# Kernel optimization log

Hardware: AMD Instinct MI355X
Metric: run time of the kernel (lower is better)

## Reference

```python
import jax, jax.numpy as jnp
import numpy as np

B, S, E, H = 4, 2048, 2048, 16
D = E // H  # head_dim = 128
ROPE_BASE = 10000.0


def rope(x, base=ROPE_BASE, offset=0):
    # x: (..., seq, d) with interleaved even/odd rotation
    d = x.shape[-1]
    s = x.shape[-2]
    inv_freq = base ** (-jnp.arange(0, d, 2, dtype=jnp.float32) / d)  # (d/2,)
    pos = jnp.arange(offset, s + offset, dtype=jnp.float32)  # (s,)
    ang = pos[:, None] * inv_freq  # (s, d/2)
    sin, cos = jnp.sin(ang), jnp.cos(ang)
    xe, xo = x[..., 0::2], x[..., 1::2]
    re = xe * cos - xo * sin
    ro = xe * sin + xo * cos
    return jnp.stack([re, ro], axis=-1).reshape(x.shape)


def setup_inputs() -> dict:
    key = jax.random.key(0)
    ks = jax.random.split(key, 9)
    w = lambda k, shp: jax.random.normal(k, shp, dtype=jnp.float32) * 0.02
    return {
        "x": jax.random.normal(ks[0], (B, S, E), dtype=jnp.float32),
        "Wq": w(ks[1], (E, E)), "bq": w(ks[2], (E,)),
        "Wk": w(ks[3], (E, E)), "bk": w(ks[4], (E,)),
        "Wv": w(ks[5], (E, E)), "bv": w(ks[6], (E,)),
        "Wo": w(ks[7], (E, E)), "bo": w(ks[8], (E,)),
    }


def reference(x, Wq, bq, Wk, bk, Wv, bv, Wo, bo):
    b, s, _ = x.shape
    scale = D ** -0.5
    # torch Linear: y = x @ W.T + b
    def proj(W, bias):
        y = jnp.einsum('bse,fe->bsf', x, W) + bias
        return y.reshape(b, s, H, D).transpose(0, 2, 1, 3)  # (b, h, s, d)
    q = rope(proj(Wq, bq))
    k = rope(proj(Wk, bk))
    v = proj(Wv, bv)
    attn = jnp.einsum('bhqd,bhkd->bhqk', q, k) * scale  # (b, h, s, s)
    causal = jnp.triu(jnp.ones((s, s), dtype=bool), k=1)
    attn = jnp.where(causal, -jnp.inf, attn)
    attn_weights = jax.nn.softmax(attn, axis=-1)
    out = jnp.einsum('bhqk,bhkd->bhqd', attn_weights, v)
    out = out.transpose(0, 2, 1, 3).reshape(b, s, E)
    return jnp.einsum('bse,fe->bsf', out, Wo) + bo
```

## Files before the change

kernel.cpp:

```cpp
#include <hip/hip_runtime.h>
#include <hip/hip_bf16.h>
#include <stdint.h>

#define B_ 4
#define S_ 2048
#define E_ 2048
#define H_ 16
#define D_ 128
#define M_ (B_ * S_)

typedef unsigned short ushort_t;
typedef unsigned int uint_t;
typedef __attribute__((ext_vector_type(4))) float f32x4;
typedef __attribute__((ext_vector_type(2))) uint_t u32x2;
typedef __attribute__((ext_vector_type(8))) short bf16x8;

__device__ __forceinline__ ushort_t f2bf(float f) {
  uint_t u = __float_as_uint(f);
  u += 0x7FFFu + ((u >> 16) & 1u);
  return (ushort_t)(u >> 16);
}
__device__ __forceinline__ float bf2f(ushort_t h) {
  return __uint_as_float(((uint_t)h) << 16);
}
__device__ __forceinline__ uint_t cvt_pk_bf16(float lo, float hi) {
  uint_t r;
  asm("v_cvt_pk_bf16_f32 %0, %1, %2" : "=v"(r) : "v"(lo), "v"(hi));
  return r;
}

#define GLOAD_LDS16(gp, lp)                                   \
  __builtin_amdgcn_global_load_lds(                           \
      (__attribute__((address_space(1))) void*)(gp),          \
      (__attribute__((address_space(3))) void*)(lp), 16, 0, 0)

__global__ void f32_to_bf16(const float* __restrict__ in, ushort_t* __restrict__ out,
                            size_t n4) {
  const size_t stride = (size_t)gridDim.x * blockDim.x;
  for (size_t i = (size_t)blockIdx.x * blockDim.x + threadIdx.x; i < n4; i += stride) {
    const f32x4 f = __builtin_nontemporal_load((const f32x4*)in + i);
    u32x2 o;
    o[0] = (uint_t)f2bf(f[0]) | ((uint_t)f2bf(f[1]) << 16);
    o[1] = (uint_t)f2bf(f[2]) | ((uint_t)f2bf(f[3]) << 16);
    __builtin_nontemporal_store(o, (u32x2*)out + i);
  }
}

__global__ void rope_table(float2* __restrict__ tab) {
  const int i = blockIdx.x * 256 + threadIdx.x;
  const int s = i >> 6, p = i & 63;
  const float inv = exp2f(-0.20762050593046f * (float)p);
  float sn, cs;
  sincosf((float)s * inv, &sn, &cs);
  tab[i] = make_float2(cs, sn);
}

__global__ __launch_bounds__(256) void transpose_v(const ushort_t* __restrict__ Vp,
                                                   ushort_t* __restrict__ Vt) {
  const int b = blockIdx.z, h = blockIdx.y;
  const int s0 = blockIdx.x * 64;
  const int tid = threadIdx.x;
  __shared__ ushort_t T[64][136];
#pragma unroll
  for (int i = 0; i < 4; i++) {
    const int c = i * 256 + tid;
    const int s = c >> 4, d8 = c & 15;
    *(bf16x8*)(&T[s][d8 * 8]) =
        *(const bf16x8*)(Vp + (size_t)(b * S_ + s0 + s) * E_ + h * D_ + d8 * 8);
  }
  __syncthreads();
#pragma unroll
  for (int i = 0; i < 4; i++) {
    const int c = i * 256 + tid;
    const int d = c >> 3, s8 = c & 7;
    bf16x8 v;
#pragma unroll
    for (int j = 0; j < 8; j++) v[j] = (short)T[s8 * 8 + j][d];
    *(bf16x8*)(Vt + ((size_t)(b * H_ + h) * D_ + d) * S_ + s0 + s8 * 8) = v;
  }
}

template <int MODE>
__global__ __launch_bounds__(512, 2) void gemm8p(const ushort_t* __restrict__ A,
                                                 const ushort_t* __restrict__ Bw,
                                                 const float* __restrict__ bias,
                                                 const float2* __restrict__ tab,
                                                 void* __restrict__ Cv) {
  __shared__ __align__(16) char lds[131072];
  const int tid = threadIdx.x;
  const int w = tid >> 6, l = tid & 63, g = l >> 4, ln = l & 15;
  const int wm = w >> 2, wn = w & 3;

  const int flat = blockIdx.x;
  const int swz = (flat & 7) * 32 + (flat >> 3);
  const int m0 = (swz >> 3) * 256, n0 = (swz & 7) * 256;

  const ushort_t* Ab = A + (size_t)m0 * E_;
  const ushort_t* Bb = Bw + (size_t)n0 * E_;

  int srcRow[2], srcCc[2];
#pragma unroll
  for (int i = 0; i < 2; i++) {
    const int c = i * 512 + tid;
    const int r2 = c >> 3;
    const int j = (c & 7) ^ (r2 & 7);
    srcRow[i] = 2 * r2 + (j >> 2);
    srcCc[i] = (j & 3) * 8;
  }

  auto STAGE = [&](int t_, int mat, int kk) {
    char* dst = lds + (t_ & 1) * 65536 + mat * 32768 + kk * 16384;
    const ushort_t* src = mat ? Bb : Ab;
#pragma unroll
    for (int i = 0; i < 2; i++)
      GLOAD_LDS16(src + (size_t)srcRow[i] * E_ + t_ * 64 + kk * 32 + srcCc[i],
                  dst + (i * 512 + w * 64) * 16);
  };

  const int rp = ln >> 1;
  const int chunkl = ((((ln & 1) << 2) | g) ^ rp);
  const int aBase = wm * 8192 + rp * 128 + chunkl * 16;
  const int bBase = 32768 + wn * 4096 + rp * 128 + chunkl * 16;

  f32x4 acc[8][4];
#pragma unroll
  for (int mi = 0; mi < 8; mi++)
#pragma unroll
    for (int ni = 0; ni < 4; ni++)
#pragma unroll
      for (int r = 0; r < 4; r++) acc[mi][ni][r] = 0.f;

#define BARR asm volatile("s_barrier" ::: "memory")
#define VM6 asm volatile("s_waitcnt vmcnt(6)" ::: "memory")
#define VM0 asm volatile("s_waitcnt vmcnt(0)" ::: "memory")
#define LGKM0                                            \
  do {                                                   \
    asm volatile("s_waitcnt lgkmcnt(0)" ::: "memory");   \
    __builtin_amdgcn_sched_barrier(0);                   \
  } while (0)
#define PH_RDB(bp, kk)                                                         \
  _Pragma("unroll") for (int ni = 0; ni < 4; ni++) bfr[ni] =                   \
      *(const bf16x8*)((bp) + bBase + (kk)*16384 + ni * 1024);
#define PH_RDA(bp, kk, mh)                                                     \
  _Pragma("unroll") for (int ai = 0; ai < 4; ai++) af[ai] =                    \
      *(const bf16x8*)((bp) + aBase + (kk)*16384 + (mh)*4096 + ai * 1024);
#define PH_MM(mh)                                                              \
  __builtin_amdgcn_s_setprio(1);                                               \
  _Pragma("unroll") for (int ai = 0; ai < 4; ai++)                             \
      _Pragma("unroll") for (int ni = 0; ni < 4; ni++) acc[(mh)*4 + ai][ni] =  \
          __builtin_amdgcn_mfma_f32_16x16x32_bf16(af[ai], bfr[ni],             \
                                                  acc[(mh)*4 + ai][ni], 0, 0, 0); \
  __builtin_amdgcn_s_setprio(0);

  STAGE(0, 1, 0); STAGE(0, 0, 0); STAGE(0, 1, 1); STAGE(0, 0, 1);
  STAGE(1, 1, 0); STAGE(1, 0, 0); STAGE(1, 1, 1);
  VM6;
  BARR;

  const char* b0 = lds;
  const char* b1 = lds + 65536;
  bf16x8 af[4], bfr[4];

  for (int it = 0; it < 15; ++it) {
    const int t2 = 2 * it;
    PH_RDB(b0, 0); PH_RDA(b0, 0, 0); STAGE(t2 + 1, 0, 1); BARR; LGKM0; PH_MM(0); BARR;
    PH_RDA(b0, 0, 1);                STAGE(t2 + 2, 1, 0); BARR; LGKM0; PH_MM(1); BARR;
    PH_RDB(b0, 1); PH_RDA(b0, 1, 0); STAGE(t2 + 2, 0, 0); BARR; LGKM0; PH_MM(0); BARR;
    PH_RDA(b0, 1, 1);                STAGE(t2 + 2, 1, 1); BARR; LGKM0; PH_MM(1); VM6; BARR;
    PH_RDB(b1, 0); PH_RDA(b1, 0, 0); STAGE(t2 + 2, 0, 1); BARR; LGKM0; PH_MM(0); BARR;
    PH_RDA(b1, 0, 1);                STAGE(t2 + 3, 1, 0); BARR; LGKM0; PH_MM(1); BARR;
    PH_RDB(b1, 1); PH_RDA(b1, 1, 0); STAGE(t2 + 3, 0, 0); BARR; LGKM0; PH_MM(0); BARR;
    PH_RDA(b1, 1, 1);                STAGE(t2 + 3, 1, 1); BARR; LGKM0; PH_MM(1); VM6; BARR;
  }
  PH_RDB(b0, 0); PH_RDA(b0, 0, 0); STAGE(31, 0, 1); BARR; LGKM0; PH_MM(0); BARR;
  PH_RDA(b0, 0, 1);                                 BARR; LGKM0; PH_MM(1); BARR;
  PH_RDB(b0, 1); PH_RDA(b0, 1, 0);                  BARR; LGKM0; PH_MM(0); BARR;
  PH_RDA(b0, 1, 1);                                 BARR; LGKM0; PH_MM(1); VM0; BARR;
  PH_RDB(b1, 0); PH_RDA(b1, 0, 0);                  BARR; LGKM0; PH_MM(0); BARR;
  PH_RDA(b1, 0, 1);                                 BARR; LGKM0; PH_MM(1); BARR;
  PH_RDB(b1, 1); PH_RDA(b1, 1, 0);                  BARR; LGKM0; PH_MM(0); BARR;
  PH_RDA(b1, 1, 1);                                 BARR; LGKM0; PH_MM(1);

#undef PH_MM
#undef PH_RDA
#undef PH_RDB
#undef LGKM0
#undef VM0
#undef VM6
#undef BARR

  float bv[4];
#pragma unroll
  for (int ni = 0; ni < 4; ni++) bv[ni] = bias[n0 + wn * 64 + ni * 16 + ln];
#pragma unroll
  for (int mi = 0; mi < 8; mi++)
#pragma unroll
    for (int ni = 0; ni < 4; ni++) {
      const int col = n0 + wn * 64 + ni * 16 + ln;
      const int p = (col & 127) >> 1;
      const float sgn = (col & 1) ? 1.f : -1.f;
      const int row0 = m0 + wm * 128 + mi * 16 + g * 4;
#pragma unroll
      for (int r = 0; r < 4; r++) {
        const float v = acc[mi][ni][r] + bv[ni];
        if (MODE == 1) {
          ((float*)Cv)[(size_t)(row0 + r) * E_ + col] = v;
        } else if (MODE == 2) {
          const float partner = __shfl_xor(v, 1);
          const float2 t = tab[((row0 + r) & (S_ - 1)) * 64 + p];
          ((ushort_t*)Cv)[(size_t)(row0 + r) * E_ + col] =
              f2bf(v * t.x + sgn * partner * t.y);
        } else {
          ((ushort_t*)Cv)[(size_t)(row0 + r) * E_ + col] = f2bf(v);
        }
      }
    }
}

__global__ __launch_bounds__(256, 2) void attn_fwd(const ushort_t* __restrict__ Q,
                                                   const ushort_t* __restrict__ K,
                                                   const ushort_t* __restrict__ Vt,
                                                   ushort_t* __restrict__ O) {
  const int flat = blockIdx.x;
  const int pair = flat >> 6;
  const int bh = flat & 63;
  const int b = bh >> 4, h = bh & 15;
  const int tid = threadIdx.x;
  const int w = tid >> 6, l = tid & 63, g = l >> 4, ln = l & 15;

  __shared__ ushort_t Ks[2][64 * 128];
  __shared__ ushort_t Vs[2][128 * 64];
  __shared__ ushort_t Ps[4][32 * 64];

  const ushort_t* Kb = K + (size_t)(b * S_) * E_ + h * D_;
  const ushort_t* Vb = Vt + (size_t)(b * H_ + h) * D_ * S_;
  const float scale = 0.08838834764831845f;

#define STAGE_KV(buf, kv0_)                                                      \
  do {                                                                           \
    _Pragma("unroll") for (int i = 0; i < 4; i++) {                              \
      const int c = i * 256 + tid;                                               \
      const int row = c >> 4, sl = c & 15;                                       \
      const int gs = sl ^ (row & 7);                                             \
      GLOAD_LDS16(Kb + (size_t)((kv0_) + row) * E_ + gs * 8,                     \
                  (char*)(&Ks[buf][0]) + (i * 256 + w * 64) * 16);               \
    }                                                                            \
    _Pragma("unroll") for (int i = 0; i < 4; i++) {                              \
      const int c = i * 256 + tid;                                               \
      const int row = c >> 3, sl = c & 7;                                        \
      const int gs = sl ^ (row & 7);                                             \
      GLOAD_LDS16(Vb + (size_t)row * S_ + (kv0_) + gs * 8,                       \
                  (char*)(&Vs[buf][0]) + (i * 256 + w * 64) * 16);               \
    }                                                                            \
  } while (0)

  for (int pass = 0; pass < 2; pass++) {
    const int u = (pass == 0) ? pair : (15 - pair);
    const int q0 = u * 128;
    const int wrow0 = q0 + w * 32;

    bf16x8 qf[2][4];
    {
      const ushort_t* qb = Q + (size_t)(b * S_ + wrow0) * E_ + h * D_;
#pragma unroll
      for (int mi = 0; mi < 2; mi++)
#pragma unroll
        for (int kk = 0; kk < 4; kk++) {
          bf16x8 v = *(const bf16x8*)(qb + (size_t)(mi * 16 + ln) * E_ + kk * 32 + g * 8);
#pragma unroll
          for (int j = 0; j < 8; j++) v[j] = (short)f2bf(bf2f((ushort_t)v[j]) * scale);
          qf[mi][kk] = v;
        }
    }

    f32x4 oacc[2][8];
#pragma unroll
    for (int mi = 0; mi < 2; mi++)
#pragma unroll
      for (int nd = 0; nd < 8; nd++)
#pragma unroll
        for (int r = 0; r < 4; r++) oacc[mi][nd][r] = 0.f;
    float mrun[2], srun[2];
#pragma unroll
    for (int mi = 0; mi < 2; mi++) {
      mrun[mi] = -__builtin_inff();
      srun[mi] = 0.f;
    }

    const int ntu = 2 * u + 2;
    STAGE_KV(0, 0);

    for (int t = 0; t < ntu; t++) {
      const int kv0 = t * 64;
      const int cur = t & 1;
      if (t + 1 < ntu) {
        STAGE_KV(cur ^ 1, kv0 + 64);
        asm volatile("s_waitcnt vmcnt(8)" ::: "memory");
      } else {
        asm volatile("s_waitcnt vmcnt(0)" ::: "memory");
      }
      __builtin_amdgcn_s_barrier();
      __builtin_amdgcn_sched_barrier(0);

      if (kv0 <= wrow0 + 31) {
        const ushort_t* Kst = &Ks[cur][0];
        const ushort_t* Vst = &Vs[cur][0];
        f32x4 sa[2][4];
#pragma unroll
        for (int mi = 0; mi < 2; mi++)
#pragma unroll
          for (int ni = 0; ni < 4; ni++)
#pragma unroll
            for (int r = 0; r < 4; r++) sa[mi][ni][r] = 0.f;
        __builtin_amdgcn_s_setprio(1);
#pragma unroll
        for (int kk = 0; kk < 4; kk++) {
          bf16x8 kf[4];
#pragma unroll
          for (int ni = 0; ni < 4; ni++) {
            const int row = ni * 16 + ln;
            const int sl = (kk * 4 + g) ^ (row & 7);
            kf[ni] = *(const bf16x8*)(Kst + row * 128 + sl * 8);
          }
#pragma unroll
          for (int mi = 0; mi < 2; mi++)
#pragma unroll
            for (int ni = 0; ni < 4; ni++)
              sa[mi][ni] =
                  __builtin_amdgcn_mfma_f32_16x16x32_bf16(kf[ni], qf[mi][kk], sa[mi][ni], 0, 0, 0);
        }
        __builtin_amdgcn_s_setprio(0);
        if (kv0 + 63 > wrow0) {
#pragma unroll
          for (int mi = 0; mi < 2; mi++) {
            const int lim = wrow0 + mi * 16 + ln - kv0;
#pragma unroll
            for (int ni = 0; ni < 4; ni++)
#pragma unroll
              for (int r = 0; r < 4; r++)
                if (ni * 16 + g * 4 + r > lim) sa[mi][ni][r] = -__builtin_inff();
          }
        }
#pragma unroll
        for (int mi = 0; mi < 2; mi++) {
          float vmax = -__builtin_inff();
#pragma unroll
          for (int ni = 0; ni < 4; ni++)
#pragma unroll
            for (int r = 0; r < 4; r++) vmax = fmaxf(vmax, sa[mi][ni][r]);
          vmax = fmaxf(vmax, __shfl_xor(vmax, 16));
          vmax = fmaxf(vmax, __shfl_xor(vmax, 32));
          if (!__all(vmax - mrun[mi] <= 8.0f)) {
            const float mnew = fmaxf(mrun[mi], vmax);
            const float fs = __expf(mrun[mi] - mnew);
            mrun[mi] = mnew;
            srun[mi] *= fs;
#pragma unroll
            for (int nd = 0; nd < 8; nd++)
#pragma unroll
              for (int r = 0; r < 4; r++) oacc[mi][nd][r] *= fs;
          }
          const float m = mrun[mi];
          float psum = 0.f;
#pragma unroll
          for (int ni = 0; ni < 4; ni++) {
            float p0 = __expf(sa[mi][ni][0] - m);
            float p1 = __expf(sa[mi][ni][1] - m);
            float p2 = __expf(sa[mi][ni][2] - m);
            float p3 = __expf(sa[mi][ni][3] - m);
            psum += (p0 + p1) + (p2 + p3);
            const int byteW =
                (((mi * 16 + ln) * 64 + ni * 16 + g * 4) * 2) ^ ((ln & 7) << 4);
            *(uint2*)((char*)(&Ps[w][0]) + byteW) =
                make_uint2(cvt_pk_bf16(p0, p1), cvt_pk_bf16(p2, p3));
          }
          psum += __shfl_xor(psum, 16);
          psum += __shfl_xor(psum, 32);
          srun[mi] += psum;
        }
        asm volatile("s_waitcnt lgkmcnt(0)" ::: "memory");
        __builtin_amdgcn_sched_barrier(0);
        __builtin_amdgcn_s_setprio(1);
#pragma unroll
        for (int ks = 0; ks < 2; ks++) {
          bf16x8 pf[2];
#pragma unroll
          for (int mi = 0; mi < 2; mi++) {
            const int byteR =
                (((mi * 16 + ln) * 64 + ks * 32 + g * 8) * 2) ^ ((ln & 7) << 4);
            pf[mi] = *(const bf16x8*)((const char*)(&Ps[w][0]) + byteR);
          }
#pragma unroll
          for (int nd = 0; nd < 8; nd++) {
            const int row = nd * 16 + ln;
            const int sl = (ks * 4 + g) ^ (row & 7);
            const bf16x8 vf = *(const bf16x8*)(Vst + row * 64 + sl * 8);
#pragma unroll
            for (int mi = 0; mi < 2; mi++)
              oacc[mi][nd] =
                  __builtin_amdgcn_mfma_f32_16x16x32_bf16(vf, pf[mi], oacc[mi][nd], 0, 0, 0);
          }
        }
        __builtin_amdgcn_s_setprio(0);
      }
      __builtin_amdgcn_s_barrier();
    }

    {
      ushort_t* Ob = O + (size_t)(b * S_ + q0 + w * 32) * E_ + h * D_;
#pragma unroll
      for (int mi = 0; mi < 2; mi++) {
        const float inv = 1.0f / srun[mi];
#pragma unroll
        for (int nd = 0; nd < 8; nd++) {
          const uint_t lo = cvt_pk_bf16(oacc[mi][nd][0] * inv, oacc[mi][nd][1] * inv);
          const uint_t hi = cvt_pk_bf16(oacc[mi][nd][2] * inv, oacc[mi][nd][3] * inv);
          *(uint2*)(Ob + (size_t)(mi * 16 + ln) * E_ + nd * 16 + g * 4) = make_uint2(lo, hi);
        }
      }
    }
  }
#undef STAGE_KV
}

extern "C" void kernel_launch(void* const* d_in, const int* in_sizes, int n_in,
                              void* d_out, int out_size, void* d_ws, size_t ws_size,
                              hipStream_t stream) {
  const float* x = (const float*)d_in[0];
  const float* Wq = (const float*)d_in[1];
  const float* bq = (const float*)d_in[2];
  const float* Wk = (const float*)d_in[3];
  const float* bk = (const float*)d_in[4];
  const float* Wv = (const float*)d_in[5];
  const float* bv = (const float*)d_in[6];
  const float* Wo = (const float*)d_in[7];
  const float* bo = (const float*)d_in[8];
  float* out = (float*)d_out;

  ushort_t* ws = (ushort_t*)d_ws;
  const size_t SZ = (size_t)M_ * E_;
  const size_t WSZ = (size_t)E_ * E_;
  ushort_t* xb = ws;
  ushort_t* Qb = ws + SZ;
  ushort_t* Kb = ws + 2 * SZ;
  float2* tbl = (float2*)(ws + 3 * SZ);
  ushort_t* Vb = ws + 3 * SZ;
  ushort_t* Vtb = ws + 4 * SZ;
  ushort_t* Wqb = ws + 5 * SZ;
  ushort_t* Wkb = Wqb + WSZ;
  ushort_t* Wvb = Wkb + WSZ;
  ushort_t* Wob = Wvb + WSZ;
  ushort_t* Ob = xb;

  f32_to_bf16<<<2048, 256, 0, stream>>>(x, xb, SZ / 4);
  f32_to_bf16<<<1024, 256, 0, stream>>>(Wq, Wqb, WSZ / 4);
  f32_to_bf16<<<1024, 256, 0, stream>>>(Wk, Wkb, WSZ / 4);
  f32_to_bf16<<<1024, 256, 0, stream>>>(Wv, Wvb, WSZ / 4);
  f32_to_bf16<<<1024, 256, 0, stream>>>(Wo, Wob, WSZ / 4);
  rope_table<<<512, 256, 0, stream>>>(tbl);

  gemm8p<2><<<256, 512, 0, stream>>>(xb, Wqb, bq, tbl, Qb);
  gemm8p<2><<<256, 512, 0, stream>>>(xb, Wkb, bk, tbl, Kb);
  gemm8p<0><<<256, 512, 0, stream>>>(xb, Wvb, bv, nullptr, Vb);
  transpose_v<<<dim3(32, H_, B_), 256, 0, stream>>>(Vb, Vtb);

  attn_fwd<<<512, 256, 0, stream>>>(Qb, Kb, Vtb, Ob);

  gemm8p<1><<<256, 512, 0, stream>>>(Ob, Wob, bo, nullptr, (void*)out);
}
```

Baseline: 424.2 us.

## Fuse QKV projections into one GEMM launch and use exp2 softmax

Merges the three Q/K/V projection GEMMs into a single 768-block launch that treats the contiguous Wq/Wk/Wv bf16 buffers as one 6144-wide weight matrix, picking bias, output and RoPE handling per column tile. This removes two launch tails and fills the GPU with more concurrent tiles. Separately, attention folds log2(e) into the Q scale and uses the raw v_exp_f32 (exp2) instruction, rescaling the lazy-rescale threshold to match. The rope table moves to a new workspace offset so it no longer aliases the V buffer.

```diff
diff --git a/kernel.cpp b/kernel.cpp
--- a/kernel.cpp
+++ b/kernel.cpp
@@ -26,6 +26,11 @@
 __device__ __forceinline__ uint_t cvt_pk_bf16(float lo, float hi) {
   uint_t r;
   asm("v_cvt_pk_bf16_f32 %0, %1, %2" : "=v"(r) : "v"(lo), "v"(hi));
+  return r;
+}
+__device__ __forceinline__ float fexp2(float x) {
+  float r;
+  asm("v_exp_f32 %0, %1" : "=v"(r) : "v"(x));
   return r;
 }
 
@@ -80,20 +85,77 @@
   }
 }
 
-template <int MODE>
-__global__ __launch_bounds__(512, 2) void gemm8p(const ushort_t* __restrict__ A,
-                                                 const ushort_t* __restrict__ Bw,
-                                                 const float* __restrict__ bias,
-                                                 const float2* __restrict__ tab,
-                                                 void* __restrict__ Cv) {
+#define G8_BARR asm volatile("s_barrier" ::: "memory")
+#define G8_VM6 asm volatile("s_waitcnt vmcnt(6)" ::: "memory")
+#define G8_VM0 asm volatile("s_waitcnt vmcnt(0)" ::: "memory")
+#define G8_LGKM0                                         \
+  do {                                                   \
+    asm volatile("s_waitcnt lgkmcnt(0)" ::: "memory");   \
+    __builtin_amdgcn_sched_barrier(0);                   \
+  } while (0)
+#define G8_RDB(bp, kk)                                                         \
+  _Pragma("unroll") for (int ni = 0; ni < 4; ni++) bfr[ni] =                   \
+      *(const bf16x8*)((bp) + bBase + (kk)*16384 + ni * 1024);
+#define G8_RDA(bp, kk, mh)                                                     \
+  _Pragma("unroll") for (int ai = 0; ai < 4; ai++) af[ai] =                    \
+      *(const bf16x8*)((bp) + aBase + (kk)*16384 + (mh)*4096 + ai * 1024);
+#define G8_MM(mh)                                                              \
+  __builtin_amdgcn_s_setprio(1);                                               \
+  _Pragma("unroll") for (int ai = 0; ai < 4; ai++)                             \
+      _Pragma("unroll") for (int ni = 0; ni < 4; ni++) acc[(mh)*4 + ai][ni] =  \
+          __builtin_amdgcn_mfma_f32_16x16x32_bf16(af[ai], bfr[ni],             \
+                                                  acc[(mh)*4 + ai][ni], 0, 0, 0); \
+  __builtin_amdgcn_s_setprio(0);
+
+#define G8_BODY                                                                              \
+  f32x4 acc[8][4];                                                                           \
+  _Pragma("unroll") for (int mi = 0; mi < 8; mi++)                                           \
+      _Pragma("unroll") for (int ni = 0; ni < 4; ni++)                                       \
+          _Pragma("unroll") for (int r = 0; r < 4; r++) acc[mi][ni][r] = 0.f;                \
+  STAGE(0, 1, 0); STAGE(0, 0, 0); STAGE(0, 1, 1); STAGE(0, 0, 1);                            \
+  STAGE(1, 1, 0); STAGE(1, 0, 0); STAGE(1, 1, 1);                                            \
+  G8_VM6; G8_BARR;                                                                           \
+  const char* b0 = lds;                                                                      \
+  const char* b1 = lds + 65536;                                                              \
+  bf16x8 af[4], bfr[4];                                                                      \
+  for (int it = 0; it < 15; ++it) {                                                          \
+    const int t2 = 2 * it;                                                                   \
+    G8_RDB(b0, 0); G8_RDA(b0, 0, 0); STAGE(t2 + 1, 0, 1); G8_BARR; G8_LGKM0; G8_MM(0); G8_BARR; \
+    G8_RDA(b0, 0, 1);                STAGE(t2 + 2, 1, 0); G8_BARR; G8_LGKM0; G8_MM(1); G8_BARR; \
+    G8_RDB(b0, 1); G8_RDA(b0, 1, 0); STAGE(t2 + 2, 0, 0); G8_BARR; G8_LGKM0; G8_MM(0); G8_BARR; \
+    G8_RDA(b0, 1, 1);                STAGE(t2 + 2, 1, 1); G8_BARR; G8_LGKM0; G8_MM(1); G8_VM6; G8_BARR; \
+    G8_RDB(b1, 0); G8_RDA(b1, 0, 0); STAGE(t2 + 2, 0, 1); G8_BARR; G8_LGKM0; G8_MM(0); G8_BARR; \
+    G8_RDA(b1, 0, 1);                STAGE(t2 + 3, 1, 0); G8_BARR; G8_LGKM0; G8_MM(1); G8_BARR; \
+    G8_RDB(b1, 1); G8_RDA(b1, 1, 0); STAGE(t2 + 3, 0, 0); G8_BARR; G8_LGKM0; G8_MM(0); G8_BARR; \
+    G8_RDA(b1, 1, 1);                STAGE(t2 + 3, 1, 1); G8_BARR; G8_LGKM0; G8_MM(1); G8_VM6; G8_BARR; \
+  }                                                                                          \
+  G8_RDB(b0, 0); G8_RDA(b0, 0, 0); STAGE(31, 0, 1); G8_BARR; G8_LGKM0; G8_MM(0); G8_BARR;    \
+  G8_RDA(b0, 0, 1);                                 G8_BARR; G8_LGKM0; G8_MM(1); G8_BARR;    \
+  G8_RDB(b0, 1); G8_RDA(b0, 1, 0);                  G8_BARR; G8_LGKM0; G8_MM(0); G8_BARR;    \
+  G8_RDA(b0, 1, 1);                                 G8_BARR; G8_LGKM0; G8_MM(1); G8_VM0; G8_BARR; \
+  G8_RDB(b1, 0); G8_RDA(b1, 0, 0);                  G8_BARR; G8_LGKM0; G8_MM(0); G8_BARR;    \
+  G8_RDA(b1, 0, 1);                                 G8_BARR; G8_LGKM0; G8_MM(1); G8_BARR;    \
+  G8_RDB(b1, 1); G8_RDA(b1, 1, 0);                  G8_BARR; G8_LGKM0; G8_MM(0); G8_BARR;    \
+  G8_RDA(b1, 1, 1);                                 G8_BARR; G8_LGKM0; G8_MM(1);
+
+__global__ __launch_bounds__(512, 2) void gemm_qkv(const ushort_t* __restrict__ A,
+                                                   const ushort_t* __restrict__ Bw,
+                                                   const float* __restrict__ bq,
+                                                   const float* __restrict__ bk,
+                                                   const float* __restrict__ bvv,
+                                                   const float2* __restrict__ tab,
+                                                   ushort_t* __restrict__ Qo,
+                                                   ushort_t* __restrict__ Ko,
+                                                   ushort_t* __restrict__ Vo) {
   __shared__ __align__(16) char lds[131072];
   const int tid = threadIdx.x;
   const int w = tid >> 6, l = tid & 63, g = l >> 4, ln = l & 15;
   const int wm = w >> 2, wn = w & 3;
 
   const int flat = blockIdx.x;
-  const int swz = (flat & 7) * 32 + (flat >> 3);
-  const int m0 = (swz >> 3) * 256, n0 = (swz & 7) * 256;
+  const int swz = (flat & 7) * 96 + (flat >> 3);
+  const int mt = swz / 24, nt = swz % 24;
+  const int m0 = mt * 256, n0 = nt * 256;
 
   const ushort_t* Ab = A + (size_t)m0 * E_;
   const ushort_t* Bb = Bw + (size_t)n0 * E_;
@@ -122,98 +184,92 @@
   const int aBase = wm * 8192 + rp * 128 + chunkl * 16;
   const int bBase = 32768 + wn * 4096 + rp * 128 + chunkl * 16;
 
-  f32x4 acc[8][4];
+  G8_BODY
+
+  const int proj = n0 >> 11;
+  const int nc0 = n0 & 2047;
+  const float* bias = proj == 0 ? bq : (proj == 1 ? bk : bvv);
+  ushort_t* dst = proj == 0 ? Qo : (proj == 1 ? Ko : Vo);
+
+  float bv4[4];
+#pragma unroll
+  for (int ni = 0; ni < 4; ni++) bv4[ni] = bias[nc0 + wn * 64 + ni * 16 + ln];
 #pragma unroll
   for (int mi = 0; mi < 8; mi++)
 #pragma unroll
-    for (int ni = 0; ni < 4; ni++)
-#pragma unroll
-      for (int r = 0; r < 4; r++) acc[mi][ni][r] = 0.f;
-
-#define BARR asm volatile("s_barrier" ::: "memory")
-#define VM6 asm volatile("s_waitcnt vmcnt(6)" ::: "memory")
-#define VM0 asm volatile("s_waitcnt vmcnt(0)" ::: "memory")
-#define LGKM0                                            \
-  do {                                                   \
-    asm volatile("s_waitcnt lgkmcnt(0)" ::: "memory");   \
-    __builtin_amdgcn_sched_barrier(0);                   \
-  } while (0)
-#define PH_RDB(bp, kk)                                                         \
-  _Pragma("unroll") for (int ni = 0; ni < 4; ni++) bfr[ni] =                   \
-      *(const bf16x8*)((bp) + bBase + (kk)*16384 + ni * 1024);
-#define PH_RDA(bp, kk, mh)                                                     \
-  _Pragma("unroll") for (int ai = 0; ai < 4; ai++) af[ai] =                    \
-      *(const bf16x8*)((bp) + aBase + (kk)*16384 + (mh)*4096 + ai * 1024);
-#define PH_MM(mh)                                                              \
-  __builtin_amdgcn_s_setprio(1);                                               \
-  _Pragma("unroll") for (int ai = 0; ai < 4; ai++)                             \
-      _Pragma("unroll") for (int ni = 0; ni < 4; ni++) acc[(mh)*4 + ai][ni] =  \
-          __builtin_amdgcn_mfma_f32_16x16x32_bf16(af[ai], bfr[ni],             \
-                                                  acc[(mh)*4 + ai][ni], 0, 0, 0); \
-  __builtin_amdgcn_s_setprio(0);
-
-  STAGE(0, 1, 0); STAGE(0, 0, 0); STAGE(0, 1, 1); STAGE(0, 0, 1);
-  STAGE(1, 1, 0); STAGE(1, 0, 0); STAGE(1, 1, 1);
-  VM6;
-  BARR;
-
-  const char* b0 = lds;
-  const char* b1 = lds + 65536;
-  bf16x8 af[4], bfr[4];
-
-  for (int it = 0; it < 15; ++it) {
-    const int t2 = 2 * it;
-    PH_RDB(b0, 0); PH_RDA(b0, 0, 0); STAGE(t2 + 1, 0, 1); BARR; LGKM0; PH_MM(0); BARR;
-    PH_RDA(b0, 0, 1);                STAGE(t2 + 2, 1, 0); BARR; LGKM0; PH_MM(1); BARR;
-    PH_RDB(b0, 1); PH_RDA(b0, 1, 0); STAGE(t2 + 2, 0, 0); BARR; LGKM0; PH_MM(0); BARR;
-    PH_RDA(b0, 1, 1);                STAGE(t2 + 2, 1, 1); BARR; LGKM0; PH_MM(1); VM6; BARR;
-    PH_RDB(b1, 0); PH_RDA(b1, 0, 0); STAGE(t2 + 2, 0, 1); BARR; LGKM0; PH_MM(0); BARR;
-    PH_RDA(b1, 0, 1);                STAGE(t2 + 3, 1, 0); BARR; LGKM0; PH_MM(1); BARR;
-    PH_RDB(b1, 1); PH_RDA(b1, 1, 0); STAGE(t2 + 3, 0, 0); BARR; LGKM0; PH_MM(0); BARR;
-    PH_RDA(b1, 1, 1);                STAGE(t2 + 3, 1, 1); BARR; LGKM0; PH_MM(1); VM6; BARR;
-  }
-  PH_RDB(b0, 0); PH_RDA(b0, 0, 0); STAGE(31, 0, 1); BARR; LGKM0; PH_MM(0); BARR;
-  PH_RDA(b0, 0, 1);                                 BARR; LGKM0; PH_MM(1); BARR;
-  PH_RDB(b0, 1); PH_RDA(b0, 1, 0);                  BARR; LGKM0; PH_MM(0); BARR;
-  PH_RDA(b0, 1, 1);                                 BARR; LGKM0; PH_MM(1); VM0; BARR;
-  PH_RDB(b1, 0); PH_RDA(b1, 0, 0);                  BARR; LGKM0; PH_MM(0); BARR;
-  PH_RDA(b1, 0, 1);                                 BARR; LGKM0; PH_MM(1); BARR;
-  PH_RDB(b1, 1); PH_RDA(b1, 1, 0);                  BARR; LGKM0; PH_MM(0); BARR;
-  PH_RDA(b1, 1, 1);                                 BARR; LGKM0; PH_MM(1);
-
-#undef PH_MM
-#undef PH_RDA
-#undef PH_RDB
-#undef LGKM0
-#undef VM0
-#undef VM6
-#undef BARR
-
-  float bv[4];
-#pragma unroll
-  for (int ni = 0; ni < 4; ni++) bv[ni] = bias[n0 + wn * 64 + ni * 16 + ln];
-#pragma unroll
-  for (int mi = 0; mi < 8; mi++)
-#pragma unroll
     for (int ni = 0; ni < 4; ni++) {
-      const int col = n0 + wn * 64 + ni * 16 + ln;
+      const int col = nc0 + wn * 64 + ni * 16 + ln;
       const int p = (col & 127) >> 1;
       const float sgn = (col & 1) ? 1.f : -1.f;
       const int row0 = m0 + wm * 128 + mi * 16 + g * 4;
 #pragma unroll
       for (int r = 0; r < 4; r++) {
-        const float v = acc[mi][ni][r] + bv[ni];
-        if (MODE == 1) {
-          ((float*)Cv)[(size_t)(row0 + r) * E_ + col] = v;
-        } else if (MODE == 2) {
+        const float v = acc[mi][ni][r] + bv4[ni];
+        if (proj < 2) {
           const float partner = __shfl_xor(v, 1);
           const float2 t = tab[((row0 + r) & (S_ - 1)) * 64 + p];
-          ((ushort_t*)Cv)[(size_t)(row0 + r) * E_ + col] =
-              f2bf(v * t.x + sgn * partner * t.y);
+          dst[(size_t)(row0 + r) * E_ + col] = f2bf(v * t.x + sgn * partner * t.y);
         } else {
-          ((ushort_t*)Cv)[(size_t)(row0 + r) * E_ + col] = f2bf(v);
+          dst[(size_t)(row0 + r) * E_ + col] = f2bf(v);
         }
       }
+    }
+}
+
+__global__ __launch_bounds__(512, 2) void gemm_out(const ushort_t* __restrict__ A,
+                                                   const ushort_t* __restrict__ Bw,
+                                                   const float* __restrict__ bias,
+                                                   float* __restrict__ Cv) {
+  __shared__ __align__(16) char lds[131072];
+  const int tid = threadIdx.x;
+  const int w = tid >> 6, l = tid & 63, g = l >> 4, ln = l & 15;
+  const int wm = w >> 2, wn = w & 3;
+
+  const int flat = blockIdx.x;
+  const int swz = (flat & 7) * 32 + (flat >> 3);
+  const int m0 = (swz >> 3) * 256, n0 = (swz & 7) * 256;
+
+  const ushort_t* Ab = A + (size_t)m0 * E_;
+  const ushort_t* Bb = Bw + (size_t)n0 * E_;
+
+  int srcRow[2], srcCc[2];
+#pragma unroll
+  for (int i = 0; i < 2; i++) {
+    const int c = i * 512 + tid;
+    const int r2 = c >> 3;
+    const int j = (c & 7) ^ (r2 & 7);
+    srcRow[i] = 2 * r2 + (j >> 2);
+    srcCc[i] = (j & 3) * 8;
+  }
+
+  auto STAGE = [&](int t_, int mat, int kk) {
+    char* dst = lds + (t_ & 1) * 65536 + mat * 32768 + kk * 16384;
+    const ushort_t* src = mat ? Bb : Ab;
+#pragma unroll
+    for (int i = 0; i < 2; i++)
+      GLOAD_LDS16(src + (size_t)srcRow[i] * E_ + t_ * 64 + kk * 32 + srcCc[i],
+                  dst + (i * 512 + w * 64) * 16);
+  };
+
+  const int rp = ln >> 1;
+  const int chunkl = ((((ln & 1) << 2) | g) ^ rp);
+  const int aBase = wm * 8192 + rp * 128 + chunkl * 16;
+  const int bBase = 32768 + wn * 4096 + rp * 128 + chunkl * 16;
+
+  G8_BODY
+
+  float bv4[4];
+#pragma unroll
+  for (int ni = 0; ni < 4; ni++) bv4[ni] = bias[n0 + wn * 64 + ni * 16 + ln];
+#pragma unroll
+  for (int mi = 0; mi < 8; mi++)
+#pragma unroll
+    for (int ni = 0; ni < 4; ni++) {
+      const int col = n0 + wn * 64 + ni * 16 + ln;
+      const int row0 = m0 + wm * 128 + mi * 16 + g * 4;
+#pragma unroll
+      for (int r = 0; r < 4; r++)
+        Cv[(size_t)(row0 + r) * E_ + col] = acc[mi][ni][r] + bv4[ni];
     }
 }
 
@@ -234,7 +290,7 @@
 
   const ushort_t* Kb = K + (size_t)(b * S_) * E_ + h * D_;
   const ushort_t* Vb = Vt + (size_t)(b * H_ + h) * D_ * S_;
-  const float scale = 0.08838834764831845f;
+  const float scale2 = 0.12751744528276693f;
 
 #define STAGE_KV(buf, kv0_)                                                      \
   do {                                                                           \
@@ -268,7 +324,7 @@
         for (int kk = 0; kk < 4; kk++) {
           bf16x8 v = *(const bf16x8*)(qb + (size_t)(mi * 16 + ln) * E_ + kk * 32 + g * 8);
 #pragma unroll
-          for (int j = 0; j < 8; j++) v[j] = (short)f2bf(bf2f((ushort_t)v[j]) * scale);
+          for (int j = 0; j < 8; j++) v[j] = (short)f2bf(bf2f((ushort_t)v[j]) * scale2);
           qf[mi][kk] = v;
         }
     }
@@ -350,9 +406,9 @@
             for (int r = 0; r < 4; r++) vmax = fmaxf(vmax, sa[mi][ni][r]);
           vmax = fmaxf(vmax, __shfl_xor(vmax, 16));
           vmax = fmaxf(vmax, __shfl_xor(vmax, 32));
-          if (!__all(vmax - mrun[mi] <= 8.0f)) {
+          if (!__all(vmax - mrun[mi] <= 11.5f)) {
             const float mnew = fmaxf(mrun[mi], vmax);
-            const float fs = __expf(mrun[mi] - mnew);
+            const float fs = fexp2(mrun[mi] - mnew);
             mrun[mi] = mnew;
             srun[mi] *= fs;
 #pragma unroll
@@ -364,10 +420,10 @@
           float psum = 0.f;
 #pragma unroll
           for (int ni = 0; ni < 4; ni++) {
-            float p0 = __expf(sa[mi][ni][0] - m);
-            float p1 = __expf(sa[mi][ni][1] - m);
-            float p2 = __expf(sa[mi][ni][2] - m);
-            float p3 = __expf(sa[mi][ni][3] - m);
+            float p0 = fexp2(sa[mi][ni][0] - m);
+            float p1 = fexp2(sa[mi][ni][1] - m);
+            float p2 = fexp2(sa[mi][ni][2] - m);
+            float p3 = fexp2(sa[mi][ni][3] - m);
             psum += (p0 + p1) + (p2 + p3);
             const int byteW =
                 (((mi * 16 + ln) * 64 + ni * 16 + g * 4) * 2) ^ ((ln & 7) << 4);
@@ -443,13 +499,13 @@
   ushort_t* xb = ws;
   ushort_t* Qb = ws + SZ;
   ushort_t* Kb = ws + 2 * SZ;
-  float2* tbl = (float2*)(ws + 3 * SZ);
   ushort_t* Vb = ws + 3 * SZ;
   ushort_t* Vtb = ws + 4 * SZ;
   ushort_t* Wqb = ws + 5 * SZ;
   ushort_t* Wkb = Wqb + WSZ;
   ushort_t* Wvb = Wkb + WSZ;
   ushort_t* Wob = Wvb + WSZ;
+  float2* tbl = (float2*)(ws + 6 * SZ);
   ushort_t* Ob = xb;
 
   f32_to_bf16<<<2048, 256, 0, stream>>>(x, xb, SZ / 4);
@@ -459,12 +515,10 @@
   f32_to_bf16<<<1024, 256, 0, stream>>>(Wo, Wob, WSZ / 4);
   rope_table<<<512, 256, 0, stream>>>(tbl);
 
-  gemm8p<2><<<256, 512, 0, stream>>>(xb, Wqb, bq, tbl, Qb);
-  gemm8p<2><<<256, 512, 0, stream>>>(xb, Wkb, bk, tbl, Kb);
-  gemm8p<0><<<256, 512, 0, stream>>>(xb, Wvb, bv, nullptr, Vb);
+  gemm_qkv<<<768, 512, 0, stream>>>(xb, Wqb, bq, bk, bv, tbl, Qb, Kb, Vb);
   transpose_v<<<dim3(32, H_, B_), 256, 0, stream>>>(Vb, Vtb);
 
   attn_fwd<<<512, 256, 0, stream>>>(Qb, Kb, Vtb, Ob);
 
-  gemm8p<1><<<256, 512, 0, stream>>>(Ob, Wob, bo, nullptr, (void*)out);
-}
+  gemm_out<<<256, 512, 0, stream>>>(Ob, Wob, bo, out);
+}
```

After: 483.4 us. 1.14x slower.
